# Kernel optimization log

Hardware: AMD Instinct MI355X
Metric: run time of the kernel (lower is better)

The kernel has to match this reference:

```python
import jax, jax.numpy as jnp
import numpy as np

B, C, H, W = 4, 3, 256, 256
NCC = 64            # num_conv_channels
N_HIDDEN = 20 - 2   # hidden_block applied num_hiddel_blocks-2 times (shared weights)
EPS = 1e-5          # BatchNorm eps (eval mode: running stats; Dropout2d is identity in eval)


def _bayer_mask():
    # RGGB Bayer pattern: each channel sampled only at its sites, zeros elsewhere
    m = np.zeros((3, H, W), dtype=np.float32)
    m[0, 0::2, 0::2] = 1.0  # R
    m[1, 0::2, 1::2] = 1.0  # G
    m[1, 1::2, 0::2] = 1.0  # G
    m[2, 1::2, 1::2] = 1.0  # B
    return jnp.asarray(m)


def setup_inputs() -> dict:
    key = jax.random.key(0)
    ks = jax.random.split(key, 8)
    X = jax.random.uniform(ks[0], (B, C, H, W), dtype=jnp.float32) * _bayer_mask()[None]
    w_in = jax.random.normal(ks[1], (NCC, 3, 3, 3), dtype=jnp.float32) * 0.15
    b_in = jnp.zeros((NCC,), jnp.float32)
    w_h = jax.random.normal(ks[2], (NCC, NCC, 3, 3), dtype=jnp.float32) * 0.04
    b_h = jnp.zeros((NCC,), jnp.float32)
    w_out = jax.random.normal(ks[3], (3, NCC, 3, 3), dtype=jnp.float32) * 0.04
    b_out = jnp.zeros((3,), jnp.float32)
    def bn_params(n):
        return (jnp.ones((n,), jnp.float32), jnp.zeros((n,), jnp.float32),
                jnp.zeros((n,), jnp.float32), jnp.ones((n,), jnp.float32))
    g_in, be_in, m_in, v_in = bn_params(NCC)
    g_h, be_h, m_h, v_h = bn_params(NCC)
    g_out, be_out, m_out, v_out = bn_params(3)
    return dict(X=X, w_in=w_in, b_in=b_in, g_in=g_in, be_in=be_in, m_in=m_in, v_in=v_in,
                w_h=w_h, b_h=b_h, g_h=g_h, be_h=be_h, m_h=m_h, v_h=v_h,
                w_out=w_out, b_out=b_out, g_out=g_out, be_out=be_out, m_out=m_out, v_out=v_out)


def _conv(x, w, b):
    y = jax.lax.conv_general_dilated(x, w, (1, 1), ((1, 1), (1, 1)),
                                     dimension_numbers=('NCHW', 'OIHW', 'NCHW'))
    return y + b[None, :, None, None]


def _bn(x, g, be, m, v):
    scale = (g / jnp.sqrt(v + EPS))[None, :, None, None]
    return (x - m[None, :, None, None]) * scale + be[None, :, None, None]


def _interpolate_zeros(x):
    # Vectorized masked cross-neighbor average at zero sites, dividing by the
    # count of strictly-positive neighbors (zero-padded borders).
    p = jnp.pad(x, ((0, 0), (0, 0), (1, 1), (1, 1)))
    left = p[:, :, 1:-1, :-2]
    right = p[:, :, 1:-1, 2:]
    top = p[:, :, :-2, 1:-1]
    bottom = p[:, :, 2:, 1:-1]
    nb_sum = left + right + top + bottom
    nb_cnt = ((left > 0).astype(x.dtype) + (right > 0).astype(x.dtype)
              + (top > 0).astype(x.dtype) + (bottom > 0).astype(x.dtype))
    mean = jnp.where(nb_cnt > 0, nb_sum / jnp.maximum(nb_cnt, 1.0), 0.0)
    return jnp.where(x == 0, mean, x)


def reference(X, w_in, b_in, g_in, be_in, m_in, v_in,
              w_h, b_h, g_h, be_h, m_h, v_h,
              w_out, b_out, g_out, be_out, m_out, v_out):
    y = jax.nn.selu(_bn(_conv(X, w_in, b_in), g_in, be_in, m_in, v_in))

    def hidden(y, _):
        y = jax.nn.selu(_bn(_conv(y, w_h, b_h), g_h, be_h, m_h, v_h))
        return y, None

    y, _ = jax.lax.scan(hidden, y, None, length=N_HIDDEN)
    y = jax.nn.selu(_bn(_conv(y, w_out, b_out), g_out, be_out, m_out, v_out))
    return y + _interpolate_zeros(X)
```

## Files before the change

kernel.cpp:

```cpp
#include <hip/hip_runtime.h>

#define EPS 1e-5f
#define SELU_L 1.0507009873554805f
#define SELU_A 1.6732632423543772f
#define SELU_LA (SELU_L * SELU_A)

typedef _Float16 half8 __attribute__((ext_vector_type(8)));
typedef _Float16 half4 __attribute__((ext_vector_type(4)));
typedef float floatx4 __attribute__((ext_vector_type(4)));

__device__ __forceinline__ float selu_f(float x) {
    return x > 0.f ? SELU_L * x : SELU_LA * (__expf(x) - 1.f);
}

__device__ __forceinline__ void gload_lds16(const _Float16* g, _Float16* l) {
    __builtin_amdgcn_global_load_lds(
        (const __attribute__((address_space(1))) void*)g,
        (__attribute__((address_space(3))) void*)l, 16, 0, 0);
}

__global__ __launch_bounds__(256) void k_prep(
    const float* __restrict__ w_h, const float* __restrict__ w_in,
    const float* __restrict__ w_out, _Float16* __restrict__ wb_h,
    _Float16* __restrict__ wb_in, _Float16* __restrict__ wb_out,
    _Float16* __restrict__ zp)
{
    int i = blockIdx.x * 256 + threadIdx.x;
    if (i < 32) zp[i] = (_Float16)0.f;
    if (i < 36864) {
        int t = i >> 11;
        int rem = i & 2047;
        int mi = rem >> 9;
        int L = (rem >> 3) & 63;
        int j = i & 7;
        int co = mi * 16 + (L & 15);
        int ci = ((t & 1) << 5) + ((L >> 4) << 3) + j;
        int s = t >> 1;
        wb_h[i] = (_Float16)w_h[(co * 64 + ci) * 9 + s];
    } else if (i < 36864 + 2048) {
        int e = i - 36864;
        int mi = e >> 9;
        int L = (e >> 3) & 63;
        int j = e & 7;
        int co = mi * 16 + (L & 15);
        int k = ((L >> 4) << 3) + j;
        _Float16 val = (_Float16)0.f;
        if (k < 27) {
            int s = k / 3, ci = k - s * 3;
            val = (_Float16)w_in[(co * 3 + ci) * 9 + s];
        }
        wb_in[e] = val;
    } else if (i < 36864 + 2048 + 9216) {
        int e = i - 36864 - 2048;
        int t = e >> 9;
        int L = (e >> 3) & 63;
        int j = e & 7;
        int co = L & 15;
        int ci = ((t & 1) << 5) + ((L >> 4) << 3) + j;
        int s = t >> 1;
        _Float16 val = (_Float16)0.f;
        if (co < 3) val = (_Float16)w_out[(co * 64 + ci) * 9 + s];
        wb_out[e] = val;
    }
}

__global__ __launch_bounds__(256) void k_conv_in_mfma(
    const float* __restrict__ X, const _Float16* __restrict__ wb,
    const float* __restrict__ bconv, const float* __restrict__ g,
    const float* __restrict__ be, const float* __restrict__ bm,
    const float* __restrict__ bv, _Float16* __restrict__ dst)
{
    __shared__ float s_x[3][18][18];
    __shared__ float s_sc[64], s_bs[64];
    const int tid = threadIdx.x;
    const int w0 = blockIdx.x * 16, h0 = blockIdx.y * 16, b = blockIdx.z;

    if (tid < 64) {
        float sc = g[tid] * rsqrtf(bv[tid] + EPS);
        s_sc[tid] = sc;
        s_bs[tid] = (bconv[tid] - bm[tid]) * sc + be[tid];
    }
    for (int idx = tid; idx < 3 * 324; idx += 256) {
        int ci = idx / 324, rem = idx - ci * 324;
        int r = rem / 18, c = rem - r * 18;
        int gh = h0 - 1 + r, gw = w0 - 1 + c;
        float val = 0.f;
        if ((unsigned)gh < 256u && (unsigned)gw < 256u)
            val = X[((b * 3 + ci) << 16) + (gh << 8) + gw];
        s_x[ci][r][c] = val;
    }
    __syncthreads();

    const int wv = tid >> 6, L = tid & 63, quad = L >> 4, l15 = L & 15;
    half8 a[4];
    #pragma unroll
    for (int mi = 0; mi < 4; ++mi)
        a[mi] = *(const half8*)(wb + (mi * 64 + L) * 8);

    floatx4 acc[4][4];
    #pragma unroll
    for (int mi = 0; mi < 4; ++mi)
        #pragma unroll
        for (int ni = 0; ni < 4; ++ni) acc[mi][ni] = (floatx4){0.f, 0.f, 0.f, 0.f};

    #pragma unroll
    for (int ni = 0; ni < 4; ++ni) {
        half8 bfr;
        #pragma unroll
        for (int j = 0; j < 8; ++j) {
            int k = quad * 8 + j;
            float xv = 0.f;
            if (k < 27) {
                int s = k / 3, ci = k - s * 3;
                int kh = s / 3, kw = s - kh * 3;
                xv = s_x[ci][wv * 4 + ni + kh][l15 + kw];
            }
            bfr[j] = (_Float16)xv;
        }
        #pragma unroll
        for (int mi = 0; mi < 4; ++mi)
            acc[mi][ni] = __builtin_amdgcn_mfma_f32_16x16x32_f16(a[mi], bfr, acc[mi][ni], 0, 0, 0);
    }

    _Float16* db = dst + ((size_t)b << 22);
    #pragma unroll
    for (int mi = 0; mi < 4; ++mi) {
        const int cob = mi * 16 + quad * 4;
        floatx4 sc = *(const floatx4*)(&s_sc[cob]);
        floatx4 bs = *(const floatx4*)(&s_bs[cob]);
        #pragma unroll
        for (int ni = 0; ni < 4; ++ni) {
            half4 ov;
            #pragma unroll
            for (int r = 0; r < 4; ++r)
                ov[r] = (_Float16)selu_f(acc[mi][ni][r] * sc[r] + bs[r]);
            const int row = h0 + wv * 4 + ni, col = w0 + l15;
            *(half4*)(db + ((((row << 8) + col) << 6) + cob)) = ov;
        }
    }
}

__global__ __launch_bounds__(512, 2) void k_hidden_v6(
    const _Float16* __restrict__ src, const _Float16* __restrict__ wb,
    const float* __restrict__ bconv, const float* __restrict__ g,
    const float* __restrict__ be, const float* __restrict__ bm,
    const float* __restrict__ bv, const _Float16* __restrict__ zp,
    _Float16* __restrict__ dst)
{
    __shared__ _Float16 s_w[36864];
    __shared__ _Float16 s_act[2][20992];
    __shared__ float s_sc[64], s_bs[64];
    const int tid = threadIdx.x;
    const int wv = tid >> 6, L = tid & 63, quad = L >> 4, l15 = L & 15;
    const int rq = wv >> 1, mh = wv & 1;

    if (tid < 64) {
        float sc = g[tid] * rsqrtf(bv[tid] + EPS);
        s_sc[tid] = sc;
        s_bs[tid] = (bconv[tid] - bm[tid]) * sc + be[tid];
    }

    #pragma unroll
    for (int k = 0; k < 9; ++k) {
        const int wc = k * 8 + wv;
        gload_lds16(wb + ((wc << 6) + L) * 8, &s_w[wc << 9]);
    }

    auto stage = [&](int tau, int buf) {
        const int b = tau >> 8, rem = tau & 255;
        const int h0 = (rem >> 4) << 4, w0 = (rem & 15) << 4;
        const _Float16* sb = src + ((size_t)b << 22);
        #pragma unroll
        for (int k = 0; k < 6; ++k) {
            const int wc = k * 8 + wv;
            if (wc < 41) {
                const int p = (wc << 3) + (L >> 3);
                const int sd = (L & 7) ^ (p & 7);
                const int rp = p / 18, cl = p - rp * 18;
                const int gh = h0 - 1 + rp, gw = w0 - 1 + cl;
                const _Float16* gp = (p < 324 && (unsigned)gh < 256u && (unsigned)gw < 256u)
                    ? sb + ((((gh << 8) + gw) << 6) + (sd << 3)) : zp;
                gload_lds16(gp, &s_act[buf][wc << 9]);
            }
        }
    };

    const int tau0 = blockIdx.x << 2;
    stage(tau0, 0);
    __syncthreads();

    for (int ti = 0; ti < 4; ++ti) {
        const int tau = tau0 + ti, cur = ti & 1;
        if (ti < 3) stage(tau + 1, cur ^ 1);

        floatx4 acc[2][4];
        #pragma unroll
        for (int m = 0; m < 2; ++m)
            #pragma unroll
            for (int ni = 0; ni < 4; ++ni) acc[m][ni] = (floatx4){0.f, 0.f, 0.f, 0.f};

        const _Float16* bufp = &s_act[cur][0];
        #pragma unroll
        for (int h = 0; h < 2; ++h) {
            const int sb8 = (h << 2) + quad;
            #pragma unroll
            for (int kw = 0; kw < 3; ++kw) {
                half8 ac[3][2];
                #pragma unroll
                for (int kh = 0; kh < 3; ++kh) {
                    const int t = ((kh * 3 + kw) << 1) + h;
                    ac[kh][0] = *(const half8*)(&s_w[((t * 4 + mh * 2 + 0) * 64 + L) * 8]);
                    ac[kh][1] = *(const half8*)(&s_w[((t * 4 + mh * 2 + 1) * 64 + L) * 8]);
                }
                #pragma unroll
                for (int j = 0; j < 6; ++j) {
                    const int p = (rq * 4 + j) * 18 + l15 + kw;
                    half8 bfr = *(const half8*)(bufp + (p << 6) + (((p & 7) ^ sb8) << 3));
                    #pragma unroll
                    for (int kh = 0; kh < 3; ++kh) {
                        const int ni = j - kh;
                        if (ni >= 0 && ni < 4) {
                            acc[0][ni] = __builtin_amdgcn_mfma_f32_16x16x32_f16(ac[kh][0], bfr, acc[0][ni], 0, 0, 0);
                            acc[1][ni] = __builtin_amdgcn_mfma_f32_16x16x32_f16(ac[kh][1], bfr, acc[1][ni], 0, 0, 0);
                        }
                    }
                }
            }
        }

        const int b = tau >> 8, rem = tau & 255;
        const int h0 = (rem >> 4) << 4, w0 = (rem & 15) << 4;
        _Float16* db = dst + ((size_t)b << 22);
        #pragma unroll
        for (int m = 0; m < 2; ++m) {
            const int cob = (mh * 2 + m) * 16 + quad * 4;
            floatx4 sc = *(const floatx4*)(&s_sc[cob]);
            floatx4 bs = *(const floatx4*)(&s_bs[cob]);
            #pragma unroll
            for (int ni = 0; ni < 4; ++ni) {
                half4 ov;
                #pragma unroll
                for (int r = 0; r < 4; ++r)
                    ov[r] = (_Float16)selu_f(acc[m][ni][r] * sc[r] + bs[r]);
                const int row = h0 + rq * 4 + ni, col = w0 + l15;
                *(half4*)(db + ((((row << 8) + col) << 6) + cob)) = ov;
            }
        }
        __syncthreads();
    }
}

__global__ __launch_bounds__(256) void k_conv_out_mfma(
    const _Float16* __restrict__ src, const _Float16* __restrict__ wb,
    const float* __restrict__ bconv, const float* __restrict__ g,
    const float* __restrict__ be, const float* __restrict__ bm,
    const float* __restrict__ bv, const float* __restrict__ X,
    float* __restrict__ out)
{
    __shared__ _Float16 s_in[324 * 72];
    const int tid = threadIdx.x;
    const int w0 = blockIdx.x * 16, h0 = blockIdx.y * 16, b = blockIdx.z;
    const _Float16* sb = src + ((size_t)b << 22);

    for (int idx = tid; idx < 2592; idx += 256) {
        int r = idx / 144, cpos = idx - r * 144;
        int col = cpos >> 3, sub = cpos & 7;
        int gh = h0 - 1 + r, gw = w0 - 1 + col;
        half8 val = {0, 0, 0, 0, 0, 0, 0, 0};
        if ((unsigned)gh < 256u && (unsigned)gw < 256u)
            val = *(const half8*)(sb + ((((gh << 8) + gw) << 6) + (sub << 3)));
        *(half8*)(&s_in[(r * 18 + col) * 72 + (sub << 3)]) = val;
    }
    __syncthreads();

    const int wv = tid >> 6, L = tid & 63, quad = L >> 4, l15 = L & 15;
    floatx4 acc[4];
    #pragma unroll
    for (int ni = 0; ni < 4; ++ni) acc[ni] = (floatx4){0.f, 0.f, 0.f, 0.f};

    #pragma unroll
    for (int t = 0; t < 18; ++t) {
        const int s = t >> 1, ci0 = (t & 1) << 5;
        const int kh = s / 3, kw = s - kh * 3;
        half8 a = *(const half8*)(wb + (t * 64 + L) * 8);
        #pragma unroll
        for (int ni = 0; ni < 4; ++ni) {
            const int row = wv * 4 + ni + kh, col = l15 + kw;
            half8 bfr = *(const half8*)(&s_in[(row * 18 + col) * 72 + ci0 + quad * 8]);
            acc[ni] = __builtin_amdgcn_mfma_f32_16x16x32_f16(a, bfr, acc[ni], 0, 0, 0);
        }
    }

    if (quad == 0) {
        float sc[3], bs[3];
        #pragma unroll
        for (int co = 0; co < 3; ++co) {
            sc[co] = g[co] * rsqrtf(bv[co] + EPS);
            bs[co] = (bconv[co] - bm[co]) * sc[co] + be[co];
        }
        #pragma unroll
        for (int ni = 0; ni < 4; ++ni) {
            const int h = h0 + wv * 4 + ni, wc = w0 + l15;
            #pragma unroll
            for (int co = 0; co < 3; ++co) {
                float val = selu_f(acc[ni][co] * sc[co] + bs[co]);
                const float* Xc = X + ((size_t)(b * 3 + co) << 16);
                float x = Xc[(h << 8) + wc];
                float res;
                if (x == 0.f) {
                    float lft = (wc > 0)   ? Xc[(h << 8) + wc - 1] : 0.f;
                    float rgt = (wc < 255) ? Xc[(h << 8) + wc + 1] : 0.f;
                    float top = (h > 0)    ? Xc[((h - 1) << 8) + wc] : 0.f;
                    float bot = (h < 255)  ? Xc[((h + 1) << 8) + wc] : 0.f;
                    float sm = lft + rgt + top + bot;
                    int cnt = (lft > 0.f) + (rgt > 0.f) + (top > 0.f) + (bot > 0.f);
                    res = cnt > 0 ? sm / (float)cnt : 0.f;
                } else {
                    res = x;
                }
                out[((b * 3 + co) << 16) + (h << 8) + wc] = val + res;
            }
        }
    }
}

extern "C" void kernel_launch(void* const* d_in, const int* in_sizes, int n_in,
                              void* d_out, int out_size, void* d_ws, size_t ws_size,
                              hipStream_t stream) {
    (void)in_sizes; (void)n_in; (void)out_size; (void)ws_size;
    const float* X    = (const float*)d_in[0];
    const float* w_in = (const float*)d_in[1];
    const float* b_in = (const float*)d_in[2];
    const float* g_in = (const float*)d_in[3];
    const float* be_in= (const float*)d_in[4];
    const float* m_in = (const float*)d_in[5];
    const float* v_in = (const float*)d_in[6];
    const float* w_h  = (const float*)d_in[7];
    const float* b_h  = (const float*)d_in[8];
    const float* g_h  = (const float*)d_in[9];
    const float* be_h = (const float*)d_in[10];
    const float* m_h  = (const float*)d_in[11];
    const float* v_h  = (const float*)d_in[12];
    const float* w_o  = (const float*)d_in[13];
    const float* b_o  = (const float*)d_in[14];
    const float* g_o  = (const float*)d_in[15];
    const float* be_o = (const float*)d_in[16];
    const float* m_o  = (const float*)d_in[17];
    const float* v_o  = (const float*)d_in[18];
    float* out = (float*)d_out;

    _Float16* act0  = (_Float16*)d_ws;
    _Float16* act1  = act0 + ((size_t)1 << 24);
    _Float16* wb_h  = act1 + ((size_t)1 << 24);
    _Float16* wb_in = wb_h + 36864;
    _Float16* wb_out= wb_in + 2048;
    _Float16* zp    = wb_out + 9216;

    dim3 grid(16, 16, 4), block(256);
    k_prep<<<188, 256, 0, stream>>>(w_h, w_in, w_o, wb_h, wb_in, wb_out, zp);
    k_conv_in_mfma<<<grid, block, 0, stream>>>(X, wb_in, b_in, g_in, be_in, m_in, v_in, act0);
    _Float16* src = act0;
    _Float16* dst = act1;
    for (int i = 0; i < 18; ++i) {
        k_hidden_v6<<<256, 512, 0, stream>>>(src, wb_h, b_h, g_h, be_h, m_h, v_h, zp, dst);
        _Float16* t = src; src = dst; dst = t;
    }
    k_conv_out_mfma<<<grid, block, 0, stream>>>(src, wb_out, b_o, g_o, be_o, m_o, v_o, X, out);
}
```

Baseline: 612.6 us.

## Fuse all hidden conv layers into one persistent kernel with grid barrier

Replaces the 18 separate hidden-layer launches with a single persistent kernel of 256 blocks. Blocks loop over the layers, ping-pong between the two activation buffers, and synchronise through an atomic counter grid barrier that k_prep resets. The aim is to remove per-launch overhead and to load the weights into LDS only once. It relies on all 256 blocks being co-resident, otherwise the spin barrier deadlocks, and inter-block visibility rests on threadfence plus atomics. After 18 layers the result sits in act0, which the output conv reads.

```diff
diff --git a/kernel.cpp b/kernel.cpp
--- a/kernel.cpp
+++ b/kernel.cpp
@@ -23,9 +23,10 @@
     const float* __restrict__ w_h, const float* __restrict__ w_in,
     const float* __restrict__ w_out, _Float16* __restrict__ wb_h,
     _Float16* __restrict__ wb_in, _Float16* __restrict__ wb_out,
-    _Float16* __restrict__ zp)
+    _Float16* __restrict__ zp, unsigned* __restrict__ bar)
 {
     int i = blockIdx.x * 256 + threadIdx.x;
+    if (i == 0) *bar = 0u;
     if (i < 32) zp[i] = (_Float16)0.f;
     if (i < 36864) {
         int t = i >> 11;
@@ -140,12 +141,13 @@
     }
 }
 
-__global__ __launch_bounds__(512, 2) void k_hidden_v6(
-    const _Float16* __restrict__ src, const _Float16* __restrict__ wb,
+__global__ __launch_bounds__(512, 2) void k_hidden_all(
+    _Float16* __restrict__ act0, _Float16* __restrict__ act1,
+    const _Float16* __restrict__ wb,
     const float* __restrict__ bconv, const float* __restrict__ g,
     const float* __restrict__ be, const float* __restrict__ bm,
     const float* __restrict__ bv, const _Float16* __restrict__ zp,
-    _Float16* __restrict__ dst)
+    unsigned* __restrict__ bar)
 {
     __shared__ _Float16 s_w[36864];
     __shared__ _Float16 s_act[2][20992];
@@ -166,10 +168,12 @@
         gload_lds16(wb + ((wc << 6) + L) * 8, &s_w[wc << 9]);
     }
 
-    auto stage = [&](int tau, int buf) {
+    const int tau0 = blockIdx.x << 2;
+
+    auto stage = [&](const _Float16* sp, int tau, int buf) {
         const int b = tau >> 8, rem = tau & 255;
         const int h0 = (rem >> 4) << 4, w0 = (rem & 15) << 4;
-        const _Float16* sb = src + ((size_t)b << 22);
+        const _Float16* sb = sp + ((size_t)b << 22);
         #pragma unroll
         for (int k = 0; k < 6; ++k) {
             const int wc = k * 8 + wv;
@@ -185,68 +189,88 @@
         }
     };
 
-    const int tau0 = blockIdx.x << 2;
-    stage(tau0, 0);
+    _Float16* src = act0;
+    _Float16* dst = act1;
+
+    stage(src, tau0, 0);
     __syncthreads();
 
-    for (int ti = 0; ti < 4; ++ti) {
-        const int tau = tau0 + ti, cur = ti & 1;
-        if (ti < 3) stage(tau + 1, cur ^ 1);
-
-        floatx4 acc[2][4];
-        #pragma unroll
-        for (int m = 0; m < 2; ++m)
-            #pragma unroll
-            for (int ni = 0; ni < 4; ++ni) acc[m][ni] = (floatx4){0.f, 0.f, 0.f, 0.f};
-
-        const _Float16* bufp = &s_act[cur][0];
-        #pragma unroll
-        for (int h = 0; h < 2; ++h) {
-            const int sb8 = (h << 2) + quad;
-            #pragma unroll
-            for (int kw = 0; kw < 3; ++kw) {
-                half8 ac[3][2];
+    for (int layer = 0; layer < 18; ++layer) {
+        for (int ti = 0; ti < 4; ++ti) {
+            const int tau = tau0 + ti, cur = ti & 1;
+            if (ti < 3) stage(src, tau + 1, cur ^ 1);
+
+            floatx4 acc[2][4];
+            #pragma unroll
+            for (int m = 0; m < 2; ++m)
                 #pragma unroll
-                for (int kh = 0; kh < 3; ++kh) {
-                    const int t = ((kh * 3 + kw) << 1) + h;
-                    ac[kh][0] = *(const half8*)(&s_w[((t * 4 + mh * 2 + 0) * 64 + L) * 8]);
-                    ac[kh][1] = *(const half8*)(&s_w[((t * 4 + mh * 2 + 1) * 64 + L) * 8]);
-                }
+                for (int ni = 0; ni < 4; ++ni) acc[m][ni] = (floatx4){0.f, 0.f, 0.f, 0.f};
+
+            const _Float16* bufp = &s_act[cur][0];
+            #pragma unroll
+            for (int h = 0; h < 2; ++h) {
+                const int sb8 = (h << 2) + quad;
                 #pragma unroll
-                for (int j = 0; j < 6; ++j) {
-                    const int p = (rq * 4 + j) * 18 + l15 + kw;
-                    half8 bfr = *(const half8*)(bufp + (p << 6) + (((p & 7) ^ sb8) << 3));
+                for (int kw = 0; kw < 3; ++kw) {
+                    half8 ac[3][2];
                     #pragma unroll
                     for (int kh = 0; kh < 3; ++kh) {
-                        const int ni = j - kh;
-                        if (ni >= 0 && ni < 4) {
-                            acc[0][ni] = __builtin_amdgcn_mfma_f32_16x16x32_f16(ac[kh][0], bfr, acc[0][ni], 0, 0, 0);
-                            acc[1][ni] = __builtin_amdgcn_mfma_f32_16x16x32_f16(ac[kh][1], bfr, acc[1][ni], 0, 0, 0);
+                        const int t = ((kh * 3 + kw) << 1) + h;
+                        ac[kh][0] = *(const half8*)(&s_w[((t * 4 + mh * 2 + 0) * 64 + L) * 8]);
+                        ac[kh][1] = *(const half8*)(&s_w[((t * 4 + mh * 2 + 1) * 64 + L) * 8]);
+                    }
+                    #pragma unroll
+                    for (int j = 0; j < 6; ++j) {
+                        const int p = (rq * 4 + j) * 18 + l15 + kw;
+                        half8 bfr = *(const half8*)(bufp + (p << 6) + (((p & 7) ^ sb8) << 3));
+                        #pragma unroll
+                        for (int kh = 0; kh < 3; ++kh) {
+                            const int ni = j - kh;
+                            if (ni >= 0 && ni < 4) {
+                                acc[0][ni] = __builtin_amdgcn_mfma_f32_16x16x32_f16(ac[kh][0], bfr, acc[0][ni], 0, 0, 0);
+                                acc[1][ni] = __builtin_amdgcn_mfma_f32_16x16x32_f16(ac[kh][1], bfr, acc[1][ni], 0, 0, 0);
+                            }
                         }
                     }
                 }
             }
-        }
-
-        const int b = tau >> 8, rem = tau & 255;
-        const int h0 = (rem >> 4) << 4, w0 = (rem & 15) << 4;
-        _Float16* db = dst + ((size_t)b << 22);
-        #pragma unroll
-        for (int m = 0; m < 2; ++m) {
-            const int cob = (mh * 2 + m) * 16 + quad * 4;
-            floatx4 sc = *(const floatx4*)(&s_sc[cob]);
-            floatx4 bs = *(const floatx4*)(&s_bs[cob]);
-            #pragma unroll
-            for (int ni = 0; ni < 4; ++ni) {
-                half4 ov;
+
+            const int b = tau >> 8, rem = tau & 255;
+            const int h0 = (rem >> 4) << 4, w0 = (rem & 15) << 4;
+            _Float16* db = dst + ((size_t)b << 22);
+            #pragma unroll
+            for (int m = 0; m < 2; ++m) {
+                const int cob = (mh * 2 + m) * 16 + quad * 4;
+                floatx4 sc = *(const floatx4*)(&s_sc[cob]);
+                floatx4 bs = *(const floatx4*)(&s_bs[cob]);
                 #pragma unroll
-                for (int r = 0; r < 4; ++r)
-                    ov[r] = (_Float16)selu_f(acc[m][ni][r] * sc[r] + bs[r]);
-                const int row = h0 + rq * 4 + ni, col = w0 + l15;
-                *(half4*)(db + ((((row << 8) + col) << 6) + cob)) = ov;
-            }
-        }
-        __syncthreads();
+                for (int ni = 0; ni < 4; ++ni) {
+                    half4 ov;
+                    #pragma unroll
+                    for (int r = 0; r < 4; ++r)
+                        ov[r] = (_Float16)selu_f(acc[m][ni][r] * sc[r] + bs[r]);
+                    const int row = h0 + rq * 4 + ni, col = w0 + l15;
+                    *(half4*)(db + ((((row << 8) + col) << 6) + cob)) = ov;
+                }
+            }
+            if (ti < 3) __syncthreads();
+        }
+
+        if (layer < 17) {
+            __syncthreads();
+            if (tid == 0) {
+                __threadfence();
+                atomicAdd(bar, 1u);
+                const unsigned tgt = 256u * (unsigned)(layer + 1);
+                while (atomicAdd(bar, 0u) < tgt) {}
+                __threadfence();
+            }
+            __syncthreads();
+
+            _Float16* t = src; src = dst; dst = t;
+            stage(src, tau0, 0);
+            __syncthreads();
+        }
     }
 }
 
@@ -355,15 +379,11 @@
     _Float16* wb_in = wb_h + 36864;
     _Float16* wb_out= wb_in + 2048;
     _Float16* zp    = wb_out + 9216;
+    unsigned* bar   = (unsigned*)(zp + 32);
 
     dim3 grid(16, 16, 4), block(256);
-    k_prep<<<188, 256, 0, stream>>>(w_h, w_in, w_o, wb_h, wb_in, wb_out, zp);
+    k_prep<<<188, 256, 0, stream>>>(w_h, w_in, w_o, wb_h, wb_in, wb_out, zp, bar);
     k_conv_in_mfma<<<grid, block, 0, stream>>>(X, wb_in, b_in, g_in, be_in, m_in, v_in, act0);
-    _Float16* src = act0;
-    _Float16* dst = act1;
-    for (int i = 0; i < 18; ++i) {
-        k_hidden_v6<<<256, 512, 0, stream>>>(src, wb_h, b_h, g_h, be_h, m_h, v_h, zp, dst);
-        _Float16* t = src; src = dst; dst = t;
-    }
-    k_conv_out_mfma<<<grid, block, 0, stream>>>(src, wb_out, b_o, g_o, be_o, m_o, v_o, X, out);
-}
+    k_hidden_all<<<256, 512, 0, stream>>>(act0, act1, wb_h, b_h, g_h, be_h, m_h, v_h, zp, bar);
+    k_conv_out_mfma<<<grid, block, 0, stream>>>(act0, wb_out, b_o, g_o, be_o, m_o, v_o, X, out);
+}
```

Result: slower. 1.014 ms (+65.5%).

## Load hidden-conv activations directly from global, drop LDS staging

Applied to the files above, without the earlier changes.

The hidden conv kernel no longer stages activation halo tiles into LDS with double buffering. Each lane now reads its B fragments straight from global memory (relying on L1/L2 for reuse across kw/kh), with bounds masks redirecting out-of-range reads to a zero page. LDS use drops to the weights only, so launch bounds allow 4 blocks per CU. The grid doubles to 512 blocks of 2 tiles each, and BN scale/bias are recomputed per lane from global. The cost is many more redundant global loads with no explicit prefetch, which trades LDS traffic and barriers for higher occupancy and cache pressure.

```diff
diff --git a/kernel.cpp b/kernel.cpp
--- a/kernel.cpp
+++ b/kernel.cpp
@@ -26,7 +26,7 @@
     _Float16* __restrict__ zp)
 {
     int i = blockIdx.x * 256 + threadIdx.x;
-    if (i < 32) zp[i] = (_Float16)0.f;
+    if (i < 256) zp[i] = (_Float16)0.f;
     if (i < 36864) {
         int t = i >> 11;
         int rem = i & 2047;
@@ -140,7 +140,7 @@
     }
 }
 
-__global__ __launch_bounds__(512, 2) void k_hidden_v6(
+__global__ __launch_bounds__(512, 4) void k_hidden_v8(
     const _Float16* __restrict__ src, const _Float16* __restrict__ wb,
     const float* __restrict__ bconv, const float* __restrict__ g,
     const float* __restrict__ be, const float* __restrict__ bm,
@@ -148,50 +148,36 @@
     _Float16* __restrict__ dst)
 {
     __shared__ _Float16 s_w[36864];
-    __shared__ _Float16 s_act[2][20992];
-    __shared__ float s_sc[64], s_bs[64];
     const int tid = threadIdx.x;
     const int wv = tid >> 6, L = tid & 63, quad = L >> 4, l15 = L & 15;
     const int rq = wv >> 1, mh = wv & 1;
 
-    if (tid < 64) {
-        float sc = g[tid] * rsqrtf(bv[tid] + EPS);
-        s_sc[tid] = sc;
-        s_bs[tid] = (bconv[tid] - bm[tid]) * sc + be[tid];
-    }
-
     #pragma unroll
     for (int k = 0; k < 9; ++k) {
         const int wc = k * 8 + wv;
         gload_lds16(wb + ((wc << 6) + L) * 8, &s_w[wc << 9]);
     }
-
-    auto stage = [&](int tau, int buf) {
+    __syncthreads();
+
+    #pragma unroll
+    for (int ti = 0; ti < 2; ++ti) {
+        const int tau = (blockIdx.x << 1) + ti;
         const int b = tau >> 8, rem = tau & 255;
         const int h0 = (rem >> 4) << 4, w0 = (rem & 15) << 4;
         const _Float16* sb = src + ((size_t)b << 22);
-        #pragma unroll
-        for (int k = 0; k < 6; ++k) {
-            const int wc = k * 8 + wv;
-            if (wc < 41) {
-                const int p = (wc << 3) + (L >> 3);
-                const int sd = (L & 7) ^ (p & 7);
-                const int rp = p / 18, cl = p - rp * 18;
-                const int gh = h0 - 1 + rp, gw = w0 - 1 + cl;
-                const _Float16* gp = (p < 324 && (unsigned)gh < 256u && (unsigned)gw < 256u)
-                    ? sb + ((((gh << 8) + gw) << 6) + (sd << 3)) : zp;
-                gload_lds16(gp, &s_act[buf][wc << 9]);
-            }
-        }
-    };
-
-    const int tau0 = blockIdx.x << 2;
-    stage(tau0, 0);
-    __syncthreads();
-
-    for (int ti = 0; ti < 4; ++ti) {
-        const int tau = tau0 + ti, cur = ti & 1;
-        if (ti < 3) stage(tau + 1, cur ^ 1);
+
+        const int r0 = h0 + rq * 4 - 1;
+        const int c0 = w0 + l15 - 1;
+        const _Float16* B0 = sb + ((ptrdiff_t)((r0 << 8) + c0) << 6) + (quad << 3);
+        const _Float16* rb[6];
+        bool rOK[6];
+        #pragma unroll
+        for (int j = 0; j < 6; ++j) {
+            rb[j] = B0 + ((ptrdiff_t)j << 14);
+            rOK[j] = (unsigned)(r0 + j) < 256u;
+        }
+        const bool cOK0 = (w0 > 0) || (l15 > 0);
+        const bool cOK2 = (w0 < 240) || (l15 < 15);
 
         floatx4 acc[2][4];
         #pragma unroll
@@ -199,10 +185,8 @@
             #pragma unroll
             for (int ni = 0; ni < 4; ++ni) acc[m][ni] = (floatx4){0.f, 0.f, 0.f, 0.f};
 
-        const _Float16* bufp = &s_act[cur][0];
         #pragma unroll
         for (int h = 0; h < 2; ++h) {
-            const int sb8 = (h << 2) + quad;
             #pragma unroll
             for (int kw = 0; kw < 3; ++kw) {
                 half8 ac[3][2];
@@ -212,30 +196,42 @@
                     ac[kh][0] = *(const half8*)(&s_w[((t * 4 + mh * 2 + 0) * 64 + L) * 8]);
                     ac[kh][1] = *(const half8*)(&s_w[((t * 4 + mh * 2 + 1) * 64 + L) * 8]);
                 }
+                half8 bfr[6];
                 #pragma unroll
                 for (int j = 0; j < 6; ++j) {
-                    const int p = (rq * 4 + j) * 18 + l15 + kw;
-                    half8 bfr = *(const half8*)(bufp + (p << 6) + (((p & 7) ^ sb8) << 3));
+                    const bool ok = rOK[j] && (kw == 0 ? cOK0 : (kw == 2 ? cOK2 : true));
+                    const _Float16* a = ok ? (rb[j] + kw * 64 + h * 32) : zp;
+                    bfr[j] = *(const half8*)a;
+                }
+                #pragma unroll
+                for (int j = 0; j < 6; ++j) {
                     #pragma unroll
                     for (int kh = 0; kh < 3; ++kh) {
                         const int ni = j - kh;
                         if (ni >= 0 && ni < 4) {
-                            acc[0][ni] = __builtin_amdgcn_mfma_f32_16x16x32_f16(ac[kh][0], bfr, acc[0][ni], 0, 0, 0);
-                            acc[1][ni] = __builtin_amdgcn_mfma_f32_16x16x32_f16(ac[kh][1], bfr, acc[1][ni], 0, 0, 0);
+                            acc[0][ni] = __builtin_amdgcn_mfma_f32_16x16x32_f16(ac[kh][0], bfr[j], acc[0][ni], 0, 0, 0);
+                            acc[1][ni] = __builtin_amdgcn_mfma_f32_16x16x32_f16(ac[kh][1], bfr[j], acc[1][ni], 0, 0, 0);
                         }
                     }
                 }
             }
         }
 
-        const int b = tau >> 8, rem = tau & 255;
-        const int h0 = (rem >> 4) << 4, w0 = (rem & 15) << 4;
         _Float16* db = dst + ((size_t)b << 22);
         #pragma unroll
         for (int m = 0; m < 2; ++m) {
             const int cob = (mh * 2 + m) * 16 + quad * 4;
-            floatx4 sc = *(const floatx4*)(&s_sc[cob]);
-            floatx4 bs = *(const floatx4*)(&s_bs[cob]);
+            floatx4 gv = *(const floatx4*)(g + cob);
+            floatx4 vv = *(const floatx4*)(bv + cob);
+            floatx4 bc = *(const floatx4*)(bconv + cob);
+            floatx4 bmv = *(const floatx4*)(bm + cob);
+            floatx4 bev = *(const floatx4*)(be + cob);
+            floatx4 sc, bs;
+            #pragma unroll
+            for (int r = 0; r < 4; ++r) {
+                sc[r] = gv[r] * rsqrtf(vv[r] + EPS);
+                bs[r] = (bc[r] - bmv[r]) * sc[r] + bev[r];
+            }
             #pragma unroll
             for (int ni = 0; ni < 4; ++ni) {
                 half4 ov;
@@ -246,7 +242,6 @@
                 *(half4*)(db + ((((row << 8) + col) << 6) + cob)) = ov;
             }
         }
-        __syncthreads();
     }
 }
 
@@ -362,7 +357,7 @@
     _Float16* src = act0;
     _Float16* dst = act1;
     for (int i = 0; i < 18; ++i) {
-        k_hidden_v6<<<256, 512, 0, stream>>>(src, wb_h, b_h, g_h, be_h, m_h, v_h, zp, dst);
+        k_hidden_v8<<<512, 512, 0, stream>>>(src, wb_h, b_h, g_h, be_h, m_h, v_h, zp, dst);
         _Float16* t = src; src = dst; dst = t;
     }
     k_conv_out_mfma<<<grid, block, 0, stream>>>(src, wb_out, b_o, g_o, be_o, m_o, v_o, X, out);
```

Result: slower. 970.6 us (+58.4%).

## Run two tile groups concurrently per 1024-thread block in hidden conv

Applied to the files above, without the earlier changes.

The hidden-layer kernel now launches 1024 threads per block, split into two groups of 8 waves that each own one activation buffer and process alternate tiles. The old sequence of four tiles with double-buffered prefetch becomes two phases in which both groups compute at once, with a restage and barrier between phases. This adds concurrent work per CU while keeping a single shared weight copy, but it gives up overlap of loading the next tile with compute and adds block-wide barriers. The zero-pad buffer initialisation is also widened.

```diff
diff --git a/kernel.cpp b/kernel.cpp
--- a/kernel.cpp
+++ b/kernel.cpp
@@ -26,7 +26,7 @@
     _Float16* __restrict__ zp)
 {
     int i = blockIdx.x * 256 + threadIdx.x;
-    if (i < 32) zp[i] = (_Float16)0.f;
+    if (i < 256) zp[i] = (_Float16)0.f;
     if (i < 36864) {
         int t = i >> 11;
         int rem = i & 2047;
@@ -140,7 +140,7 @@
     }
 }
 
-__global__ __launch_bounds__(512, 2) void k_hidden_v6(
+__global__ __launch_bounds__(1024) void k_hidden_v10(
     const _Float16* __restrict__ src, const _Float16* __restrict__ wb,
     const float* __restrict__ bconv, const float* __restrict__ g,
     const float* __restrict__ be, const float* __restrict__ bm,
@@ -152,7 +152,8 @@
     __shared__ float s_sc[64], s_bs[64];
     const int tid = threadIdx.x;
     const int wv = tid >> 6, L = tid & 63, quad = L >> 4, l15 = L & 15;
-    const int rq = wv >> 1, mh = wv & 1;
+    const int gg = wv >> 3, wg = wv & 7;
+    const int rq = wg >> 1, mh = wg & 1;
 
     if (tid < 64) {
         float sc = g[tid] * rsqrtf(bv[tid] + EPS);
@@ -161,9 +162,10 @@
     }
 
     #pragma unroll
-    for (int k = 0; k < 9; ++k) {
-        const int wc = k * 8 + wv;
-        gload_lds16(wb + ((wc << 6) + L) * 8, &s_w[wc << 9]);
+    for (int k = 0; k < 5; ++k) {
+        const int wc = k * 16 + wv;
+        if (wc < 72)
+            gload_lds16(wb + ((wc << 6) + L) * 8, &s_w[wc << 9]);
     }
 
     auto stage = [&](int tau, int buf) {
@@ -172,7 +174,7 @@
         const _Float16* sb = src + ((size_t)b << 22);
         #pragma unroll
         for (int k = 0; k < 6; ++k) {
-            const int wc = k * 8 + wv;
+            const int wc = k * 8 + wg;
             if (wc < 41) {
                 const int p = (wc << 3) + (L >> 3);
                 const int sd = (L & 7) ^ (p & 7);
@@ -185,13 +187,13 @@
         }
     };
 
-    const int tau0 = blockIdx.x << 2;
-    stage(tau0, 0);
+    const int tau_base = blockIdx.x << 2;
+    stage(tau_base + gg, gg);
     __syncthreads();
 
-    for (int ti = 0; ti < 4; ++ti) {
-        const int tau = tau0 + ti, cur = ti & 1;
-        if (ti < 3) stage(tau + 1, cur ^ 1);
+    #pragma unroll
+    for (int p = 0; p < 2; ++p) {
+        const int tau = tau_base + 2 * p + gg;
 
         floatx4 acc[2][4];
         #pragma unroll
@@ -199,7 +201,7 @@
             #pragma unroll
             for (int ni = 0; ni < 4; ++ni) acc[m][ni] = (floatx4){0.f, 0.f, 0.f, 0.f};
 
-        const _Float16* bufp = &s_act[cur][0];
+        const _Float16* bufp = &s_act[gg][0];
         #pragma unroll
         for (int h = 0; h < 2; ++h) {
             const int sb8 = (h << 2) + quad;
@@ -214,8 +216,8 @@
                 }
                 #pragma unroll
                 for (int j = 0; j < 6; ++j) {
-                    const int p = (rq * 4 + j) * 18 + l15 + kw;
-                    half8 bfr = *(const half8*)(bufp + (p << 6) + (((p & 7) ^ sb8) << 3));
+                    const int px = (rq * 4 + j) * 18 + l15 + kw;
+                    half8 bfr = *(const half8*)(bufp + (px << 6) + (((px & 7) ^ sb8) << 3));
                     #pragma unroll
                     for (int kh = 0; kh < 3; ++kh) {
                         const int ni = j - kh;
@@ -247,6 +249,11 @@
             }
         }
         __syncthreads();
+
+        if (p == 0) {
+            stage(tau + 2, gg);
+            __syncthreads();
+        }
     }
 }
 
@@ -362,7 +369,7 @@
     _Float16* src = act0;
     _Float16* dst = act1;
     for (int i = 0; i < 18; ++i) {
-        k_hidden_v6<<<256, 512, 0, stream>>>(src, wb_h, b_h, g_h, be_h, m_h, v_h, zp, dst);
+        k_hidden_v10<<<256, 1024, 0, stream>>>(src, wb_h, b_h, g_h, be_h, m_h, v_h, zp, dst);
         _Float16* t = src; src = dst; dst = t;
     }
     k_conv_out_mfma<<<grid, block, 0, stream>>>(src, wb_out, b_o, g_o, be_o, m_o, v_o, X, out);
```

Result: slower. 675.3 us (+10.2%).
